# Optimization experiments

Measured on AMD Instinct MI355X. Metric: run time of the kernel, lower is better.

The kernel has to match this reference:

```python
import jax, jax.numpy as jnp
import numpy as np

B, S, D_MODEL, N_HEADS, MAX_LEN = 2, 1024, 1024, 16, 1024
D_K = D_MODEL // N_HEADS


def setup_inputs() -> dict:
    key = jax.random.key(0)
    ks = jax.random.split(key, 8)
    w_std = 1.0 / np.sqrt(D_MODEL)  # ~ torch Linear default scale
    inp = {
        "query": jax.random.normal(ks[0], (B, S, D_MODEL), jnp.float32),
        "key": jax.random.normal(ks[1], (B, S, D_MODEL), jnp.float32),
        "value": jax.random.normal(ks[2], (B, S, D_MODEL), jnp.float32),
        "Wq": jax.random.normal(ks[3], (D_MODEL, D_MODEL), jnp.float32) * w_std,
        "Wk": jax.random.normal(ks[4], (D_MODEL, D_MODEL), jnp.float32) * w_std,
        "Wv": jax.random.normal(ks[5], (D_MODEL, D_MODEL), jnp.float32) * w_std,
        "Wo": jax.random.normal(ks[6], (D_MODEL, D_MODEL), jnp.float32) * w_std,
        "bq": jnp.zeros((D_MODEL,), jnp.float32),
        "bk": jnp.zeros((D_MODEL,), jnp.float32),
        "bv": jnp.zeros((D_MODEL,), jnp.float32),
        "bo": jnp.zeros((D_MODEL,), jnp.float32),
        "Er": jax.random.normal(ks[7], (2 * MAX_LEN - 1, D_K), jnp.float32) * 0.02,
    }
    return inp


def _rel_positions(q_len, k_len, max_len):
    pos = jnp.arange(q_len)[:, None] - jnp.arange(k_len)[None, :]
    pos = jnp.clip(pos, -max_len + 1, max_len - 1)
    return pos + max_len - 1  # [q_len, k_len] indices into Er


def reference(query, key, value, Wq, Wk, Wv, Wo, bq, bk, bv, bo, Er):
    b, q_len, d_model = query.shape
    k_len = key.shape[1]
    d_k = Er.shape[-1]
    h = d_model // d_k
    scale = 1.0 / np.sqrt(d_k)

    def proj(x, W, bias):  # torch Linear: x @ W.T + b, then split heads -> [b,h,s,d_k]
        y = x @ W.T + bias
        return y.reshape(b, -1, h, d_k).transpose(0, 2, 1, 3)

    q = proj(query, Wq, bq)
    k = proj(key, Wk, bk)
    v = proj(value, Wv, bv)

    positions = _rel_positions(q_len, k_len, MAX_LEN)  # [q,k]
    # QEr[b,h,q,k] = sum_d q[b,h,q,d] * Er[positions[q,k], d]
    # computed as a full contraction against Er then a gather on the relative axis
    qe_all = jnp.einsum('bhqd,rd->bhqr', q, Er)  # [b,h,q,2*max_len-1]
    qer = jnp.take_along_axis(qe_all, positions[None, None, :, :], axis=-1)  # [b,h,q,k]

    qk = jnp.einsum('bhqd,bhkd->bhqk', q, k)
    scores = (qk + qer) * scale
    p_attn = jax.nn.softmax(scores, axis=-1)  # dropout=0.0 (eval)
    out = jnp.einsum('bhqk,bhkd->bhqd', p_attn, v)

    out = out.transpose(0, 2, 1, 3).reshape(b, q_len, h * d_k)
    return out @ Wo.T + bo
```

## Files before the change

### kernel.cpp

```cpp
#include <hip/hip_runtime.h>
#include <hip/hip_bf16.h>
#include <cstdint>
#include <cstddef>

typedef __attribute__((ext_vector_type(8))) short bf16x8;
typedef __attribute__((ext_vector_type(4))) float f32x4;
typedef unsigned short u16;
typedef unsigned int u32;

#define DEV static __device__ __forceinline__

constexpr int Sc = 1024, DMc = 1024, Hc = 16, DKc = 64;

DEV u16 f2bf(float f) {
  u32 u = __float_as_uint(f);
  return (u16)((u + 0x7FFFu + ((u >> 16) & 1u)) >> 16);
}
DEV float bf2f(u16 h) { return __uint_as_float(((u32)h) << 16); }

#define GLDS16(g, l)                                                        \
  __builtin_amdgcn_global_load_lds(                                         \
      (const __attribute__((address_space(1))) void*)(g),                   \
      (__attribute__((address_space(3))) void*)(l), 16, 0, 0)

struct CvtJob { const float* in; u16* out; int nchunk; int rsh; int nreal; };
struct CvtArgs { CvtJob j[8]; };

__global__ __launch_bounds__(256) void cvt_kernel(CvtArgs a) {
  CvtJob job = a.j[blockIdx.y];
  int ci = (int)(blockIdx.x * 256 + threadIdx.x);
  if (ci >= job.nchunk) return;
  bf16x8 o = {};
  if (ci < job.nreal) {
    const float* src = job.in + (size_t)ci * 8;
    float4 v0 = *(const float4*)src;
    float4 v1 = *(const float4*)(src + 4);
    o[0] = (short)f2bf(v0.x); o[1] = (short)f2bf(v0.y);
    o[2] = (short)f2bf(v0.z); o[3] = (short)f2bf(v0.w);
    o[4] = (short)f2bf(v1.x); o[5] = (short)f2bf(v1.y);
    o[6] = (short)f2bf(v1.z); o[7] = (short)f2bf(v1.w);
  }
  int row = ci >> job.rsh;
  int co = (ci & ~7) | ((ci & 7) ^ (row & 7));
  *(bf16x8*)(job.out + (size_t)co * 8) = o;
}

struct GemmJob { const u16* A; const u16* W; const float* bias; void* out; };
struct GemmArgs { GemmJob p[3]; };

template<int BM, int BN, int MODE>
__global__ __launch_bounds__(256, 2) void gemm_bt(GemmArgs G) {
  constexpr int MI = BM / 32, NI = BN / 32;
  __shared__ __align__(16) u16 sA[2][BM * 64];
  __shared__ __align__(16) u16 sB[2][BN * 64];
  const int tid = threadIdx.x, lane = tid & 63, w = tid >> 6;
  const int cl = lane & 15, rg = lane >> 4;
  const int srow = lane >> 3, schk = lane & 7;
  int z, m0, n0;
  if (MODE == 0) {
    int id = blockIdx.x;
    if (id < 512) { z = id >> 8; int r = id & 255; m0 = (r >> 3) * 64; n0 = (r & 7) * 128; }
    else          { z = 2;       int r = id - 512; m0 = (r >> 4) * 64; n0 = (r & 15) * 128; }
  } else {
    z = 0; int id = blockIdx.x; m0 = (id >> 4) * 64; n0 = (id & 15) * 64;
  }
  GemmJob P = G.p[z];
  constexpr int K = 1024;
  const int wm = (w >> 1) * (BM / 2), wn = (w & 1) * (BN / 2);
  f32x4 acc[MI][NI] = {};

  auto stage = [&](int kt, int b) {
    const u16* Ab = P.A + (size_t)m0 * K + kt * 64;
    const u16* Wb = P.W + (size_t)n0 * K + kt * 64;
    #pragma unroll
    for (int i = 0; i < BM / 32; ++i)
      GLDS16(Ab + (size_t)(i * 32 + w * 8 + srow) * K + schk * 8, &sA[b][(i * 32 + w * 8) * 64]);
    #pragma unroll
    for (int i = 0; i < BN / 32; ++i)
      GLDS16(Wb + (size_t)(i * 32 + w * 8 + srow) * K + schk * 8, &sB[b][(i * 32 + w * 8) * 64]);
  };

  stage(0, 0);
  for (int kt = 0; kt < 16; ++kt) {
    __syncthreads();
    if (kt < 15) stage(kt + 1, (kt + 1) & 1);
    const u16* A_ = sA[kt & 1];
    const u16* B_ = sB[kt & 1];
    #pragma unroll
    for (int kk = 0; kk < 2; ++kk) {
      bf16x8 af[MI], bfr[NI];
      #pragma unroll
      for (int mi = 0; mi < MI; ++mi) {
        int row = wm + mi * 16 + cl;
        af[mi] = *(const bf16x8*)(A_ + row * 64 + ((kk * 4 + rg) ^ (row & 7)) * 8);
      }
      #pragma unroll
      for (int ni = 0; ni < NI; ++ni) {
        int row = wn + ni * 16 + cl;
        bfr[ni] = *(const bf16x8*)(B_ + row * 64 + ((kk * 4 + rg) ^ (row & 7)) * 8);
      }
      #pragma unroll
      for (int mi = 0; mi < MI; ++mi)
        #pragma unroll
        for (int ni = 0; ni < NI; ++ni)
          acc[mi][ni] = __builtin_amdgcn_mfma_f32_16x16x32_bf16(af[mi], bfr[ni], acc[mi][ni], 0, 0, 0);
    }
  }
  #pragma unroll
  for (int mi = 0; mi < MI; ++mi) {
    #pragma unroll
    for (int ni = 0; ni < NI; ++ni) {
      #pragma unroll
      for (int j = 0; j < 4; ++j) {
        int m = m0 + wm + mi * 16 + rg * 4 + j;
        int n = n0 + wn + ni * 16 + cl;
        if (MODE == 1) {
          ((float*)P.out)[(size_t)m * DMc + n] = acc[mi][ni][j] + P.bias[n];
        } else if (z < 2) {
          float v = acc[mi][ni][j] + P.bias[n];
          int h = n >> 6, d = n & 63;
          int c2 = (d >> 3) ^ (m & 7);
          ((u16*)P.out)[((size_t)((m >> 10) * Hc + h) * Sc + (m & 1023)) * DKc + c2 * 8 + (d & 7)] = f2bf(v);
        } else {
          float v = acc[mi][ni][j] + P.bias[m];
          int d = m & 63, h = m >> 6, bb = n >> 10, s = n & 1023;
          int c2 = ((s & 63) >> 3) ^ (d & 7);
          ((u16*)P.out)[((size_t)(bb * Hc + h) * DKc + d) * Sc + (s & ~63) + c2 * 8 + (s & 7)] = f2bf(v);
        }
      }
    }
  }
}

__global__ __launch_bounds__(256, 4) void attn_rel(
    const u16* __restrict__ qg, const u16* __restrict__ kg,
    const u16* __restrict__ vtg, const u16* __restrict__ erg,
    u16* __restrict__ Opart, float* __restrict__ lpart) {
  __shared__ __align__(16) u16 sK[64 * 64];
  __shared__ __align__(16) u16 sV[64 * 64];
  __shared__ __align__(16) u16 sU[4][1440];
  const int tid = threadIdx.x, lane = tid & 63, w = tid >> 6;
  const int cl = lane & 15, rg = lane >> 4;
  const int key = cl & 7;
  const int bh = blockIdx.x & 31, qt = (blockIdx.x >> 5) & 15, half = blockIdx.x >> 9;
  const int q0 = qt * 64, t0 = half * 8;

  const u16* qrow = qg + ((size_t)bh * Sc + q0 + w * 16 + cl) * DKc;
  bf16x8 qf0 = *(const bf16x8*)(qrow + (rg ^ key) * 8);
  bf16x8 qf1 = *(const bf16x8*)(qrow + ((rg + 4) ^ key) * 8);
  f32x4 oacc[4] = {};
  float lsum = 0.f;
  u16* Uw = sU[w];
  const u16* kbase = kg + (size_t)bh * Sc * DKc;
  const u16* vbase = vtg + (size_t)bh * DKc * Sc;

  auto stage = [&](int t) {
    const u16* ks = kbase + t * 64 * 64;
    #pragma unroll
    for (int i = 0; i < 2; ++i) {
      GLDS16(ks + (i * 32 + w * 8) * 64 + lane * 8, &sK[(i * 32 + w * 8) * 64]);
      GLDS16(vbase + (size_t)(i * 32 + w * 8 + (lane >> 3)) * Sc + t * 64 + (lane & 7) * 8,
             &sV[(i * 32 + w * 8) * 64]);
    }
  };

  stage(t0);
  for (int tt = 0; tt < 8; ++tt) {
    const int t = t0 + tt;
    __syncthreads();

    f32x4 sct[4];
    #pragma unroll
    for (int nc = 0; nc < 4; ++nc) {
      const u16* kr = sK + (nc * 16 + cl) * 64;
      bf16x8 b0 = *(const bf16x8*)(kr + (rg ^ key) * 8);
      bf16x8 b1 = *(const bf16x8*)(kr + ((rg + 4) ^ key) * 8);
      f32x4 a = {};
      a = __builtin_amdgcn_mfma_f32_16x16x32_bf16(b0, qf0, a, 0, 0, 0);
      a = __builtin_amdgcn_mfma_f32_16x16x32_bf16(b1, qf1, a, 0, 0, 0);
      sct[nc] = a;
    }
    const u16* ebase = erg + (size_t)(q0 + w * 16 - t * 64 + 960) * DKc;
    #pragma unroll
    for (int rc0 = 0; rc0 < 5; ++rc0) {
      const u16* er = ebase + (size_t)(rc0 * 16 + cl) * DKc;
      bf16x8 e0 = *(const bf16x8*)(er + (rg ^ key) * 8);
      bf16x8 e1 = *(const bf16x8*)(er + ((rg + 4) ^ key) * 8);
      f32x4 a = {};
      a = __builtin_amdgcn_mfma_f32_16x16x32_bf16(qf0, e0, a, 0, 0, 0);
      a = __builtin_amdgcn_mfma_f32_16x16x32_bf16(qf1, e1, a, 0, 0, 0);
      u16* tp = Uw + (rc0 * 16 + cl) * 18 + rg * 4;
      ushort2 lo, hi;
      lo.x = f2bf(a[0]); lo.y = f2bf(a[1]);
      hi.x = f2bf(a[2]); hi.y = f2bf(a[3]);
      *(ushort2*)tp = lo;
      *(ushort2*)(tp + 2) = hi;
    }
    float pv[4][4];
    #pragma unroll
    for (int nc = 0; nc < 4; ++nc) {
      #pragma unroll
      for (int j = 0; j < 4; ++j) {
        int r = cl + 63 - (nc * 16 + rg * 4 + j);
        float tval = bf2f(Uw[r * 18 + cl]);
        float p = __expf((sct[nc][j] + tval) * 0.125f);
        lsum += p;
        pv[nc][j] = p;
      }
    }
    #pragma unroll
    for (int nc = 0; nc < 4; ++nc) {
      ushort4 pk;
      pk.x = f2bf(pv[nc][0]); pk.y = f2bf(pv[nc][1]);
      pk.z = f2bf(pv[nc][2]); pk.w = f2bf(pv[nc][3]);
      *(ushort4*)(Uw + cl * 76 + nc * 16 + rg * 4) = pk;
    }
    bf16x8 pa0 = *(const bf16x8*)(Uw + cl * 76 + rg * 8);
    bf16x8 pa1 = *(const bf16x8*)(Uw + cl * 76 + 32 + rg * 8);
    #pragma unroll
    for (int dc = 0; dc < 4; ++dc) {
      const u16* vr = sV + (dc * 16 + cl) * 64;
      bf16x8 b0 = *(const bf16x8*)(vr + (rg ^ key) * 8);
      bf16x8 b1 = *(const bf16x8*)(vr + ((rg + 4) ^ key) * 8);
      oacc[dc] = __builtin_amdgcn_mfma_f32_16x16x32_bf16(pa0, b0, oacc[dc], 0, 0, 0);
      oacc[dc] = __builtin_amdgcn_mfma_f32_16x16x32_bf16(pa1, b1, oacc[dc], 0, 0, 0);
    }
    __syncthreads();
    if (tt < 7) stage(t + 1);
  }
  lsum += __shfl_xor(lsum, 16);
  lsum += __shfl_xor(lsum, 32);
  const size_t pb = (size_t)(half * 32 + bh) * Sc;
  if (rg == 0) lpart[pb + q0 + w * 16 + cl] = lsum;
  u16* Ob = Opart + (pb + q0 + w * 16) * DKc;
  #pragma unroll
  for (int dc = 0; dc < 4; ++dc)
    #pragma unroll
    for (int j = 0; j < 4; ++j)
      Ob[(rg * 4 + j) * DKc + dc * 16 + cl] = f2bf(oacc[dc][j]);
}

__global__ __launch_bounds__(256) void merge_kernel(
    const u16* __restrict__ O, const float* __restrict__ l,
    u16* __restrict__ attnb) {
  int ci = (int)(blockIdx.x * 256 + threadIdx.x);
  int bh = ci >> 13, rem = ci & 8191, s = rem >> 3, dc = rem & 7;
  const u16* o0 = O + ((size_t)bh * Sc + s) * DKc + dc * 8;
  const u16* o1 = o0 + (size_t)32 * Sc * DKc;
  float rinv = 1.0f / (l[(size_t)bh * Sc + s] + l[(size_t)(32 + bh) * Sc + s]);
  bf16x8 a = *(const bf16x8*)o0;
  bf16x8 b = *(const bf16x8*)o1;
  bf16x8 o;
  #pragma unroll
  for (int e = 0; e < 8; ++e)
    o[e] = (short)f2bf((bf2f((u16)a[e]) + bf2f((u16)b[e])) * rinv);
  int bb = bh >> 4, h = bh & 15;
  int c2 = dc ^ (s & 7);
  *(bf16x8*)(attnb + ((size_t)(bb * Sc + s)) * DMc + h * DKc + c2 * 8) = o;
}

extern "C" void kernel_launch(void* const* d_in, const int* in_sizes, int n_in,
                              void* d_out, int out_size, void* d_ws, size_t ws_size,
                              hipStream_t stream) {
  (void)in_sizes; (void)n_in; (void)out_size; (void)ws_size;
  const float* query = (const float*)d_in[0];
  const float* key_  = (const float*)d_in[1];
  const float* value = (const float*)d_in[2];
  const float* Wq = (const float*)d_in[3];
  const float* Wk = (const float*)d_in[4];
  const float* Wv = (const float*)d_in[5];
  const float* Wo = (const float*)d_in[6];
  const float* bq = (const float*)d_in[7];
  const float* bk = (const float*)d_in[8];
  const float* bv = (const float*)d_in[9];
  const float* bo = (const float*)d_in[10];
  const float* Er = (const float*)d_in[11];

  char* p = (char*)d_ws;
  size_t off = 0;
  auto alloc = [&](size_t bytes) {
    char* r = p + off;
    off += (bytes + 255) & ~(size_t)255;
    return r;
  };
  u16* Xq  = (u16*)alloc((size_t)2048 * 1024 * 2);
  u16* Xk  = (u16*)alloc((size_t)2048 * 1024 * 2);
  u16* Xv  = (u16*)alloc((size_t)2048 * 1024 * 2);
  u16* Wqb = (u16*)alloc((size_t)1024 * 1024 * 2);
  u16* Wkb = (u16*)alloc((size_t)1024 * 1024 * 2);
  u16* Wvb = (u16*)alloc((size_t)1024 * 1024 * 2);
  u16* Wob = (u16*)alloc((size_t)1024 * 1024 * 2);
  u16* Erb = (u16*)alloc((size_t)2048 * 64 * 2);
  u16* qh  = (u16*)alloc((size_t)2048 * 1024 * 2);
  u16* kh  = (u16*)alloc((size_t)2048 * 1024 * 2);
  u16* vt  = (u16*)alloc((size_t)2048 * 1024 * 2);
  u16* attnb = (u16*)alloc((size_t)2048 * 1024 * 2);
  u16* Opart = (u16*)alloc((size_t)2 * 32 * 1024 * 64 * 2);
  float* lpart = (float*)alloc((size_t)2 * 32 * 1024 * 4);

  CvtArgs ca;
  ca.j[0] = {query, Xq, 262144, 7, 262144};
  ca.j[1] = {key_,  Xk, 262144, 7, 262144};
  ca.j[2] = {value, Xv, 262144, 7, 262144};
  ca.j[3] = {Wq, Wqb, 131072, 7, 131072};
  ca.j[4] = {Wk, Wkb, 131072, 7, 131072};
  ca.j[5] = {Wv, Wvb, 131072, 7, 131072};
  ca.j[6] = {Wo, Wob, 131072, 7, 131072};
  ca.j[7] = {Er, Erb, 16384, 3, 16376};
  cvt_kernel<<<dim3(1024, 8, 1), 256, 0, stream>>>(ca);

  GemmArgs gp;
  gp.p[0] = {Xq, Wqb, bq, (void*)qh};
  gp.p[1] = {Xk, Wkb, bk, (void*)kh};
  gp.p[2] = {Wvb, Xv, bv, (void*)vt};
  gemm_bt<64, 128, 0><<<dim3(768, 1, 1), 256, 0, stream>>>(gp);

  attn_rel<<<dim3(1024, 1, 1), 256, 0, stream>>>(qh, kh, vt, Erb, Opart, lpart);

  merge_kernel<<<dim3(1024, 1, 1), 256, 0, stream>>>(Opart, lpart, attnb);

  GemmArgs go;
  go.p[0] = {attnb, Wob, bo, d_out};
  go.p[1] = go.p[0];
  go.p[2] = go.p[0];
  gemm_bt<64, 64, 1><<<dim3(512, 1, 1), 256, 0, stream>>>(go);
}
```

Before: 92.74 us.

## Drop split-K attention and merge kernel; normalize output inside attention kernel

The attention kernel no longer splits the key range into two halves with partial outputs. Each block now loops over all 16 key tiles, normalizes by the row sum in-kernel and writes directly into the swizzled attnb layout. The separate merge kernel and the partial O/l buffers are removed, which saves one launch and a round-trip of partial results through memory. In exchange the grid halves to 512 blocks, so there is less parallelism and each block does a longer serial loop. The scratch row stride also changes from 18 to 20 so the score tile can be written with a single 8-byte store.

```diff
diff --git a/kernel.cpp b/kernel.cpp
--- a/kernel.cpp
+++ b/kernel.cpp
@@ -135,15 +135,15 @@
 __global__ __launch_bounds__(256, 4) void attn_rel(
     const u16* __restrict__ qg, const u16* __restrict__ kg,
     const u16* __restrict__ vtg, const u16* __restrict__ erg,
-    u16* __restrict__ Opart, float* __restrict__ lpart) {
+    u16* __restrict__ og) {
   __shared__ __align__(16) u16 sK[64 * 64];
   __shared__ __align__(16) u16 sV[64 * 64];
-  __shared__ __align__(16) u16 sU[4][1440];
+  __shared__ __align__(16) u16 sU[4][1600];
   const int tid = threadIdx.x, lane = tid & 63, w = tid >> 6;
   const int cl = lane & 15, rg = lane >> 4;
   const int key = cl & 7;
-  const int bh = blockIdx.x & 31, qt = (blockIdx.x >> 5) & 15, half = blockIdx.x >> 9;
-  const int q0 = qt * 64, t0 = half * 8;
+  const int bh = blockIdx.x & 31, qt = blockIdx.x >> 5;
+  const int q0 = qt * 64;
 
   const u16* qrow = qg + ((size_t)bh * Sc + q0 + w * 16 + cl) * DKc;
   bf16x8 qf0 = *(const bf16x8*)(qrow + (rg ^ key) * 8);
@@ -164,9 +164,8 @@
     }
   };
 
-  stage(t0);
-  for (int tt = 0; tt < 8; ++tt) {
-    const int t = t0 + tt;
+  stage(0);
+  for (int t = 0; t < 16; ++t) {
     __syncthreads();
 
     f32x4 sct[4];
@@ -189,12 +188,10 @@
       f32x4 a = {};
       a = __builtin_amdgcn_mfma_f32_16x16x32_bf16(qf0, e0, a, 0, 0, 0);
       a = __builtin_amdgcn_mfma_f32_16x16x32_bf16(qf1, e1, a, 0, 0, 0);
-      u16* tp = Uw + (rc0 * 16 + cl) * 18 + rg * 4;
-      ushort2 lo, hi;
-      lo.x = f2bf(a[0]); lo.y = f2bf(a[1]);
-      hi.x = f2bf(a[2]); hi.y = f2bf(a[3]);
-      *(ushort2*)tp = lo;
-      *(ushort2*)(tp + 2) = hi;
+      ushort4 pk4;
+      pk4.x = f2bf(a[0]); pk4.y = f2bf(a[1]);
+      pk4.z = f2bf(a[2]); pk4.w = f2bf(a[3]);
+      *(ushort4*)(Uw + (rc0 * 16 + cl) * 20 + rg * 4) = pk4;
     }
     float pv[4][4];
     #pragma unroll
@@ -202,7 +199,7 @@
       #pragma unroll
       for (int j = 0; j < 4; ++j) {
         int r = cl + 63 - (nc * 16 + rg * 4 + j);
-        float tval = bf2f(Uw[r * 18 + cl]);
+        float tval = bf2f(Uw[r * 20 + cl]);
         float p = __expf((sct[nc][j] + tval) * 0.125f);
         lsum += p;
         pv[nc][j] = p;
@@ -226,37 +223,27 @@
       oacc[dc] = __builtin_amdgcn_mfma_f32_16x16x32_bf16(pa1, b1, oacc[dc], 0, 0, 0);
     }
     __syncthreads();
-    if (tt < 7) stage(t + 1);
+    if (t < 15) stage(t + 1);
   }
   lsum += __shfl_xor(lsum, 16);
   lsum += __shfl_xor(lsum, 32);
-  const size_t pb = (size_t)(half * 32 + bh) * Sc;
-  if (rg == 0) lpart[pb + q0 + w * 16 + cl] = lsum;
-  u16* Ob = Opart + (pb + q0 + w * 16) * DKc;
+  float* lw = (float*)Uw;
+  if (rg == 0) lw[cl] = lsum;
+  float linv[4];
   #pragma unroll
-  for (int dc = 0; dc < 4; ++dc)
-    #pragma unroll
-    for (int j = 0; j < 4; ++j)
-      Ob[(rg * 4 + j) * DKc + dc * 16 + cl] = f2bf(oacc[dc][j]);
-}
-
-__global__ __launch_bounds__(256) void merge_kernel(
-    const u16* __restrict__ O, const float* __restrict__ l,
-    u16* __restrict__ attnb) {
-  int ci = (int)(blockIdx.x * 256 + threadIdx.x);
-  int bh = ci >> 13, rem = ci & 8191, s = rem >> 3, dc = rem & 7;
-  const u16* o0 = O + ((size_t)bh * Sc + s) * DKc + dc * 8;
-  const u16* o1 = o0 + (size_t)32 * Sc * DKc;
-  float rinv = 1.0f / (l[(size_t)bh * Sc + s] + l[(size_t)(32 + bh) * Sc + s]);
-  bf16x8 a = *(const bf16x8*)o0;
-  bf16x8 b = *(const bf16x8*)o1;
-  bf16x8 o;
+  for (int j = 0; j < 4; ++j) linv[j] = 1.0f / lw[rg * 4 + j];
+  const int b_ = bh >> 4, h = bh & 15;
   #pragma unroll
-  for (int e = 0; e < 8; ++e)
-    o[e] = (short)f2bf((bf2f((u16)a[e]) + bf2f((u16)b[e])) * rinv);
-  int bb = bh >> 4, h = bh & 15;
-  int c2 = dc ^ (s & 7);
-  *(bf16x8*)(attnb + ((size_t)(bb * Sc + s)) * DMc + h * DKc + c2 * 8) = o;
+  for (int dc = 0; dc < 4; ++dc) {
+    #pragma unroll
+    for (int j = 0; j < 4; ++j) {
+      int qr = q0 + w * 16 + rg * 4 + j;
+      float v = oacc[dc][j] * linv[j];
+      int col = dc * 16 + cl;
+      int c2 = (col >> 3) ^ (qr & 7);
+      og[((size_t)(b_ * Sc + qr)) * DMc + h * 64 + c2 * 8 + (col & 7)] = f2bf(v);
+    }
+  }
 }
 
 extern "C" void kernel_launch(void* const* d_in, const int* in_sizes, int n_in,
@@ -295,8 +282,6 @@
   u16* kh  = (u16*)alloc((size_t)2048 * 1024 * 2);
   u16* vt  = (u16*)alloc((size_t)2048 * 1024 * 2);
   u16* attnb = (u16*)alloc((size_t)2048 * 1024 * 2);
-  u16* Opart = (u16*)alloc((size_t)2 * 32 * 1024 * 64 * 2);
-  float* lpart = (float*)alloc((size_t)2 * 32 * 1024 * 4);
 
   CvtArgs ca;
   ca.j[0] = {query, Xq, 262144, 7, 262144};
@@ -315,9 +300,7 @@
   gp.p[2] = {Wvb, Xv, bv, (void*)vt};
   gemm_bt<64, 128, 0><<<dim3(768, 1, 1), 256, 0, stream>>>(gp);
 
-  attn_rel<<<dim3(1024, 1, 1), 256, 0, stream>>>(qh, kh, vt, Erb, Opart, lpart);
-
-  merge_kernel<<<dim3(1024, 1, 1), 256, 0, stream>>>(Opart, lpart, attnb);
+  attn_rel<<<dim3(512, 1, 1), 256, 0, stream>>>(qh, kh, vt, Erb, attnb);
 
   GemmArgs go;
   go.p[0] = {attnb, Wob, bo, d_out};
```

Result: slower. 94.98 us (+2.4%).
